# Performance work log

Hardware: AMD Instinct MI355X
Metric: run time of the kernel (lower is better)

The kernel has to match this reference:

```python
import jax, jax.numpy as jnp
import numpy as np
import math

# ---- static configuration (mirrors Renderer defaults) ----
S = 129                                 # density cube side
L = math.ceil(S * math.sqrt(3))         # padded/rotation cube side = 224
C_ABS = 0.2                             # absorption coefficient c
LIGHTS = [
    {'dir': (2, 1, 1),    'rgb': (1.0, 69.0 / 255.0, 25.0 / 255.0)},
    {'dir': (-1, 0.5, 0), 'rgb': (227.0 / 255.0, 1.0, 66.0 / 255.0)},
]


def yp_from_light(l):
    ld = np.asarray(l, dtype=np.float64)
    ld = ld / np.sqrt(np.sum(ld ** 2))
    y = -math.asin(ld[0])
    if ld[2] < 0:
        y = -math.pi - y
    y = y * 180.0 / math.pi
    p = math.asin(ld[1]) * 180.0 / math.pi
    return y, p


def rot_matrix(yaw_deg, pitch_deg, order):
    # yaw about the y (height) axis, pitch about the x axis, roll = 0
    y = math.radians(yaw_deg)
    p = math.radians(pitch_deg)
    Ry = np.array([[math.cos(y), 0.0, math.sin(y)],
                   [0.0, 1.0, 0.0],
                   [-math.sin(y), 0.0, math.cos(y)]], dtype=np.float32)
    Rp = np.array([[1.0, 0.0, 0.0],
                   [0.0, math.cos(p), -math.sin(p)],
                   [0.0, math.sin(p), math.cos(p)]], dtype=np.float32)
    return Ry @ Rp if order == 'ypr' else Rp @ Ry

# base normalized sampling grid (align_corners=True convention), (x,y,z) order
_lin = np.linspace(-1.0, 1.0, L, dtype=np.float32)
_zz, _yy, _xx = np.meshgrid(_lin, _lin, _lin, indexing='ij')
BASE_XYZ = np.stack([_xx, _yy, _zz], axis=-1)   # [L,L,L,3]


def rotate_volume(vol, R):
    """Trilinear resampling of vol [B,C,D,H,W] under rotation R (zero padding)."""
    B, Ch, D, H, W = vol.shape
    src = jnp.einsum('dhwc,kc->dhwk', jnp.asarray(BASE_XYZ), jnp.asarray(R))
    xs = (src[..., 0] + 1.0) * 0.5 * (W - 1)
    ys = (src[..., 1] + 1.0) * 0.5 * (H - 1)
    zs = (src[..., 2] + 1.0) * 0.5 * (D - 1)
    x0 = jnp.floor(xs).astype(jnp.int32)
    y0 = jnp.floor(ys).astype(jnp.int32)
    z0 = jnp.floor(zs).astype(jnp.int32)
    wx = (xs - x0).astype(vol.dtype)
    wy = (ys - y0).astype(vol.dtype)
    wz = (zs - z0).astype(vol.dtype)
    flat = vol.reshape(B, Ch, D * H * W)

    def gather(zi, yi, xi):
        inb = ((zi >= 0) & (zi < D) & (yi >= 0) & (yi < H) & (xi >= 0) & (xi < W)).astype(vol.dtype)
        idx = ((jnp.clip(zi, 0, D - 1) * H + jnp.clip(yi, 0, H - 1)) * W
               + jnp.clip(xi, 0, W - 1)).reshape(-1)
        return jnp.take(flat, idx, axis=2).reshape(B, Ch, D, H, W) * inb

    out = (gather(z0,     y0,     x0)     * ((1 - wz) * (1 - wy) * (1 - wx))
         + gather(z0,     y0,     x0 + 1) * ((1 - wz) * (1 - wy) * wx)
         + gather(z0,     y0 + 1, x0)     * ((1 - wz) * wy * (1 - wx))
         + gather(z0,     y0 + 1, x0 + 1) * ((1 - wz) * wy * wx)
         + gather(z0 + 1, y0,     x0)     * (wz * (1 - wy) * (1 - wx))
         + gather(z0 + 1, y0,     x0 + 1) * (wz * (1 - wy) * wx)
         + gather(z0 + 1, y0 + 1, x0)     * (wz * wy * (1 - wx))
         + gather(z0 + 1, y0 + 1, x0 + 1) * (wz * wy * wx))
    return out


def _revcumsum(a):
    # torch.flip(cumsum(flip(a,[2]),2),[2]) : reverse cumulative sum along depth
    return jnp.flip(jnp.cumsum(jnp.flip(a, 2), axis=2), 2)


def setup_inputs() -> dict:
    key = jax.random.key(0)
    d = jax.random.uniform(key, (1, 1, S, S, S), dtype=jnp.float32)
    return {'d': d}


def reference(d):
    bs, _, Sd, _, _ = d.shape
    i = L // 2 - Sd // 2
    j = i + Sd
    light_array = jnp.zeros((bs, 3, Sd, Sd, Sd), dtype=d.dtype)
    for l in LIGHTS:
        y, p = yp_from_light(l['dir'])
        up = jnp.zeros((bs, 1, L, L, L), dtype=d.dtype).at[:, :, i:j, i:j, i:j].set(d)
        up = rotate_volume(up, rot_matrix(y, p, 'ypr'))
        up = jnp.exp(-C_ABS * _revcumsum(up))           # transmittance toward light
        up = rotate_volume(up, rot_matrix(-y, -p, 'rpy'))
        color = jnp.asarray(l['rgb'], dtype=d.dtype).reshape(1, 3, 1, 1, 1)
        light_array = light_array + up[:, :, i:j, i:j, i:j] * color
    t = jnp.exp(-C_ABS * _revcumsum(d))                  # view-ray transmittance
    out = C_ABS * jnp.sum(d * light_array * t, axis=2)   # background = 0
    return jnp.clip(out, 0.0, 1.0)
```

## Files before the change

### kernel.cpp

```cpp
#include <hip/hip_runtime.h>
#include <hip/hip_fp16.h>
#include <math.h>

#ifndef M_PI
#define M_PI 3.14159265358979323846
#endif

#define SS   129
#define LL   224
#define LL2  (LL*LL)
#define LL3  (LL*LL*LL)
#define SS2  (SS*SS)
#define SS3  (SS*SS*SS)
#define CABS 0.2f
#define PAD  48

#define BLO 45.5f
#define BHI 178.5f

#define NT1  28
#define NTZ16 14
#define ROTG  (2 * NTZ16 * 784)
#define NT3  17
#define TPL3 4913
#define NTZ  28
#define NSEG 4
#define SEGZ 33

#define RBX 21
#define RBY 16
#define RBZ 18
#define RBN (RBX*RBY*RBZ)
#define RSXZ (RBX*RBZ)

#define GLN  3584

struct Mat3 { float m[9]; };
struct F3   { float x, y, z; };

__device__ __forceinline__ F3 tile_center(const Mat3& M, int ox, int oy, int oz) {
    float cbx = fmaf((float)ox + 3.5f, 2.0f / 223.0f, -1.0f);
    float cby = fmaf((float)oy + 3.5f, 2.0f / 223.0f, -1.0f);
    float cbz = fmaf((float)oz + 3.5f, 2.0f / 223.0f, -1.0f);
    F3 qc;
    qc.x = fmaf(fmaf(M.m[0], cbx, fmaf(M.m[1], cby, M.m[2] * cbz)), 111.5f, 111.5f);
    qc.y = fmaf(fmaf(M.m[3], cbx, fmaf(M.m[4], cby, M.m[5] * cbz)), 111.5f, 111.5f);
    qc.z = fmaf(fmaf(M.m[6], cbx, fmaf(M.m[7], cby, M.m[8] * cbz)), 111.5f, 111.5f);
    return qc;
}

__device__ __forceinline__ F3 tile_center16(const Mat3& M, int ox, int oy, int oz) {
    float cbx = fmaf((float)ox + 3.5f, 2.0f / 223.0f, -1.0f);
    float cby = fmaf((float)oy + 3.5f, 2.0f / 223.0f, -1.0f);
    float cbz = fmaf((float)oz + 7.5f, 2.0f / 223.0f, -1.0f);
    F3 qc;
    qc.x = fmaf(fmaf(M.m[0], cbx, fmaf(M.m[1], cby, M.m[2] * cbz)), 111.5f, 111.5f);
    qc.y = fmaf(fmaf(M.m[3], cbx, fmaf(M.m[4], cby, M.m[5] * cbz)), 111.5f, 111.5f);
    qc.z = fmaf(fmaf(M.m[6], cbx, fmaf(M.m[7], cby, M.m[8] * cbz)), 111.5f, 111.5f);
    return qc;
}

__device__ __forceinline__ bool tile_accept(F3 qc, F3 H) {
    return !(qc.x + H.x < BLO || qc.x - H.x > BHI ||
             qc.y + H.y < BLO || qc.y - H.y > BHI ||
             qc.z + H.z < BLO || qc.z - H.z > BHI);
}

__device__ __forceinline__ void qmap(const Mat3& M, int x, int y, int z,
                                     float& qx, float& qy, float& qz) {
    float bx = fmaf((float)x, 2.0f / 223.0f, -1.0f);
    float by = fmaf((float)y, 2.0f / 223.0f, -1.0f);
    float bz = fmaf((float)z, 2.0f / 223.0f, -1.0f);
    qx = fmaf(fmaf(M.m[0], bx, fmaf(M.m[1], by, M.m[2] * bz)), 111.5f, 111.5f);
    qy = fmaf(fmaf(M.m[3], bx, fmaf(M.m[4], by, M.m[5] * bz)), 111.5f, 111.5f);
    qz = fmaf(fmaf(M.m[6], bx, fmaf(M.m[7], by, M.m[8] * bz)), 111.5f, 111.5f);
}

__device__ __forceinline__ float fetch_d(const float* __restrict__ d, int z, int y, int x) {
    unsigned zz = (unsigned)(z - PAD), yy = (unsigned)(y - PAD), xx = (unsigned)(x - PAD);
    return (zz < (unsigned)SS && yy < (unsigned)SS && xx < (unsigned)SS)
        ? d[((int)zz * SS + (int)yy) * SS + (int)xx] : 0.0f;
}

__device__ __forceinline__ float fetch_T(const float* __restrict__ T, int z, int y, int x) {
    unsigned zz = (unsigned)z, yy = (unsigned)y, xx = (unsigned)x;
    return (zz < (unsigned)LL && yy < (unsigned)LL && xx < (unsigned)LL)
        ? T[((int)zz * LL + (int)yy) * LL + (int)xx] : 0.0f;
}

__device__ __forceinline__ float tri_T(const float* __restrict__ T, float qz, float qy, float qx) {
    int x0 = (int)floorf(qx), y0 = (int)floorf(qy), z0 = (int)floorf(qz);
    float wx = qx - (float)x0, wy = qy - (float)y0, wz = qz - (float)z0;
    float c000 = fetch_T(T, z0, y0, x0),     c001 = fetch_T(T, z0, y0, x0 + 1);
    float c010 = fetch_T(T, z0, y0 + 1, x0), c011 = fetch_T(T, z0, y0 + 1, x0 + 1);
    float c100 = fetch_T(T, z0 + 1, y0, x0),     c101 = fetch_T(T, z0 + 1, y0, x0 + 1);
    float c110 = fetch_T(T, z0 + 1, y0 + 1, x0), c111 = fetch_T(T, z0 + 1, y0 + 1, x0 + 1);
    float a00 = c000 + wx * (c001 - c000), a01 = c010 + wx * (c011 - c010);
    float a10 = c100 + wx * (c101 - c100), a11 = c110 + wx * (c111 - c110);
    float b0 = a00 + wy * (a01 - a00), b1 = a10 + wy * (a11 - a10);
    return b0 + wz * (b1 - b0);
}

__device__ __forceinline__ float tri_d_g(const float* __restrict__ d, float qz, float qy, float qx) {
    int x0 = (int)floorf(qx), y0 = (int)floorf(qy), z0 = (int)floorf(qz);
    float wx = qx - (float)x0, wy = qy - (float)y0, wz = qz - (float)z0;
    float c000 = fetch_d(d, z0, y0, x0),     c001 = fetch_d(d, z0, y0, x0 + 1);
    float c010 = fetch_d(d, z0, y0 + 1, x0), c011 = fetch_d(d, z0, y0 + 1, x0 + 1);
    float c100 = fetch_d(d, z0 + 1, y0, x0),     c101 = fetch_d(d, z0 + 1, y0, x0 + 1);
    float c110 = fetch_d(d, z0 + 1, y0 + 1, x0), c111 = fetch_d(d, z0 + 1, y0 + 1, x0 + 1);
    float a00 = c000 + wx * (c001 - c000), a01 = c010 + wx * (c011 - c010);
    float a10 = c100 + wx * (c101 - c100), a11 = c110 + wx * (c111 - c110);
    float b0 = a00 + wy * (a01 - a00), b1 = a10 + wy * (a11 - a10);
    return b0 + wz * (b1 - b0);
}

__device__ __forceinline__ float tri_rot(const float* __restrict__ S,
                                         float qx, float qy, float qz,
                                         int lox, int loy, int loz) {
    int x0 = (int)floorf(qx), y0 = (int)floorf(qy), z0 = (int)floorf(qz);
    float wx = qx - (float)x0, wy = qy - (float)y0, wz = qz - (float)z0;
    int i = (y0 - loy) * 378 + (z0 - loz) * 21 + (x0 - lox);
    float c000 = S[i],        c001 = S[i + 1];
    float cz0  = S[i + 21],   cz1  = S[i + 22];
    float cy0  = S[i + 378],  cy1  = S[i + 379];
    float cw0  = S[i + 399],  cw1  = S[i + 400];
    float a00 = c000 + wx * (c001 - c000);
    float a01 = cy0  + wx * (cy1  - cy0);
    float a10 = cz0  + wx * (cz1  - cz0);
    float a11 = cw0  + wx * (cw1  - cw0);
    float b0  = a00 + wy * (a01 - a00);
    float b1  = a10 + wy * (a11 - a10);
    return b0 + wz * (b1 - b0);
}

__device__ __forceinline__ float tri_back(const float* __restrict__ S,
                                          float qx, float qy, float qz,
                                          int lox, int loy, int loz) {
    int x0 = (int)floorf(qx), y0 = (int)floorf(qy), z0 = (int)floorf(qz);
    float wx = qx - (float)x0, wy = qy - (float)y0, wz = qz - (float)z0;
    int i = ((y0 - loy) * 16 + (z0 - loz)) * 16 + (x0 - lox);
    float c000 = S[i],       c001 = S[i + 1];
    float cz0  = S[i + 16],  cz1  = S[i + 17];
    float cy0  = S[i + 256], cy1  = S[i + 257];
    float cw0  = S[i + 272], cw1  = S[i + 273];
    float a00 = c000 + wx * (c001 - c000);
    float a01 = cy0  + wx * (cy1  - cy0);
    float a10 = cz0  + wx * (cz1  - cz0);
    float a11 = cw0  + wx * (cw1  - cw0);
    float b0  = a00 + wy * (a01 - a00);
    float b1  = a10 + wy * (a11 - a10);
    return b0 + wz * (b1 - b0);
}

__global__ __launch_bounds__(256) void k_pre(const float* __restrict__ d,
        float* __restrict__ Dseg, float* __restrict__ A,
        unsigned short* __restrict__ Run, Mat3 M0, Mat3 M1, F3 H0, F3 H1) {
    int b = blockIdx.x;
    if (b < 261) {
        int t = b * 256 + threadIdx.x;
        if (t < 2 * SS2) A[t] = 0.0f;
        if (t >= NSEG * SS2) return;
        int seg = t / SS2, col = t - seg * SS2;
        int zs = seg * SEGZ, ze = min(SS, zs + SEGZ);
        float run = 0.0f;
        for (int z = zs; z < ze; ++z) run += d[z * SS2 + col];
        Dseg[t] = run;
    } else {
        int id = (b - 261) * 256 + threadIdx.x;
        if (id >= 2 * 784) return;
        int l = id / 784, r = id - l * 784;
        int ty = r / 28, tx = r - ty * 28;
        const Mat3 M = l ? M1 : M0;
        const F3  H  = l ? H1 : H0;
        int t0 = -1, t1 = -1;
        for (int tz = 0; tz < NT1; ++tz) {
            F3 qc = tile_center(M, tx * 8, ty * 8, tz * 8);
            if (tile_accept(qc, H)) { if (t0 < 0) t0 = tz; t1 = tz; }
        }
        Run[id] = (t0 < 0) ? 0xFFFFu : (unsigned short)(t0 | (t1 << 8));
    }
}

__global__ __launch_bounds__(512) void k_rot(const float* __restrict__ d,
        __half* __restrict__ T0, __half* __restrict__ T1,
        float* __restrict__ S0, float* __restrict__ S1,
        Mat3 M0, Mat3 M1, F3 H0, F3 H1) {
    int b = blockIdx.x;
    int light = b / (NTZ16 * 784);
    int r = b - light * (NTZ16 * 784);
    int tz16 = r / 784;
    int r2 = r - tz16 * 784;
    int tty = r2 / 28, ttx = r2 - tty * 28;

    const Mat3 M = light ? M1 : M0;
    const F3  H  = light ? H1 : H0;
    __half* __restrict__ T   = light ? T1 : T0;
    float* __restrict__ Ssum = light ? S1 : S0;

    int ox = ttx * 8, oy = tty * 8, oz = tz16 * 16;
    F3 qc = tile_center16(M, ox, oy, oz);
    if (!tile_accept(qc, H)) return;

    int lox = (int)floorf(qc.x - H.x);
    int loy = (int)floorf(qc.y - H.y);
    int loz = (int)floorf(qc.z - H.z);

    __shared__ float S[RBN];
    __shared__ float Sc[1024];
    int tid = threadIdx.x;

    if (tid < RSXZ) {
        int ix = tid % RBX, iz = tid / RBX;
        int lb = iz * RBX + ix;
        bool interior = (lox >= PAD) & (lox <= PAD + SS - RBX) &
                        (loy >= PAD) & (loy <= PAD + SS - RBY) &
                        (loz >= PAD) & (loz <= PAD + SS - RBZ);
        if (interior) {
            const float* g = d + ((size_t)(loz + iz - PAD) * SS + (loy - PAD)) * SS
                               + (lox + ix - PAD);
            #pragma unroll
            for (int j = 0; j < RBY; ++j)
                S[lb + j * RSXZ] = g[j * SS];
        } else {
            #pragma unroll
            for (int j = 0; j < RBY; ++j)
                S[lb + j * RSXZ] = fetch_d(d, loz + iz, loy + j, lox + ix);
        }
    }
    __syncthreads();

    int lx = tid & 7, ly = (tid >> 3) & 7, lz = tid >> 6;
    int col = tid & 63;
    float fx = (float)lx - 3.5f, fy = (float)ly - 3.5f, fz = (float)lz - 7.5f;
    float qx = qc.x + fmaf(M.m[0], fx, fmaf(M.m[1], fy, M.m[2] * fz));
    float qy = qc.y + fmaf(M.m[3], fx, fmaf(M.m[4], fy, M.m[5] * fz));
    float qz = qc.z + fmaf(M.m[6], fx, fmaf(M.m[7], fy, M.m[8] * fz));
    float v0 = tri_rot(S, qx, qy, qz, lox, loy, loz);
    float qx2 = qx + 8.0f * M.m[2];
    float qy2 = qy + 8.0f * M.m[5];
    float qz2 = qz + 8.0f * M.m[8];
    float v1 = tri_rot(S, qx2, qy2, qz2, lox, loy, loz);

    Sc[lz * 64 + col] = v0;
    Sc[(lz + 8) * 64 + col] = v1;
    __syncthreads();
    if (tid < 64) {
        int so = (oy + (tid >> 3)) * LL + (ox + (tid & 7));
        float s = 0.0f;
        #pragma unroll
        for (int k = 15; k >= 8; --k) { s += Sc[k * 64 + tid]; Sc[k * 64 + tid] = s; }
        Ssum[(2 * tz16 + 1) * LL2 + so] = s;
        float s2 = 0.0f;
        #pragma unroll
        for (int k = 7; k >= 0; --k) { s2 += Sc[k * 64 + tid]; Sc[k * 64 + tid] = s2; }
        Ssum[(2 * tz16) * LL2 + so] = s2;
    }
    __syncthreads();
    int to = (oy + ly) * LL + (ox + lx);
    T[(size_t)(oz + lz) * LL2 + to]     = __float2half(Sc[lz * 64 + col]);
    T[(size_t)(oz + 8 + lz) * LL2 + to] = __float2half(Sc[(lz + 8) * 64 + col]);
}

__global__ __launch_bounds__(256) void k_sufw(float* __restrict__ S0,
        float* __restrict__ S1, const unsigned short* __restrict__ Run,
        const float* __restrict__ d, const float* __restrict__ Dseg,
        float* __restrict__ W) {
    int b = blockIdx.x;
    if (b < 392) {
        int l = b / 196;
        int col = (b - l * 196) * 256 + threadIdx.x;
        float* __restrict__ Ssum = l ? S1 : S0;
        int x = col % LL, y = col / LL;
        unsigned short r = Run[l * 784 + (y >> 3) * 28 + (x >> 3)];
        if (r == 0xFFFFu) return;
        int t0 = r & 0xFF, t1 = r >> 8;
        float vbuf[NTZ];
        #pragma unroll
        for (int t = 0; t < NTZ; ++t)
            vbuf[t] = (t >= t0 && t <= t1) ? Ssum[t * LL2 + col] : 0.0f;
        float run = 0.0f;
        #pragma unroll
        for (int t = NTZ - 1; t >= 0; --t) {
            if (t >= t0 && t <= t1) Ssum[t * LL2 + col] = run;
            run += vbuf[t];
        }
    } else {
        int t = (b - 392) * 256 + threadIdx.x;
        if (t >= NSEG * SS2) return;
        int seg = t / SS2, col = t - seg * SS2;
        int zs = seg * SEGZ, ze = min(SS, zs + SEGZ);
        float run = 0.0f;
        for (int s2 = seg + 1; s2 < NSEG; ++s2) run += Dseg[s2 * SS2 + col];
        for (int z = ze - 1; z >= zs; --z) {
            float dv = d[z * SS2 + col];
            run += dv;
            W[z * SS2 + col] = dv * __expf(-CABS * run);
        }
    }
}

template<bool BINT>
__global__ __launch_bounds__(512) void k_back(const __half* __restrict__ T0,
        const __half* __restrict__ T1, const float* __restrict__ S0,
        const float* __restrict__ S1, const float* __restrict__ W,
        float* __restrict__ A0, float* __restrict__ A1,
        Mat3 M0, Mat3 M1, F3 H0, F3 H1) {
    int b = blockIdx.x;
    int light = b / TPL3; b -= light * TPL3;
    const Mat3 M = light ? M1 : M0;
    const F3  H  = light ? H1 : H0;
    const __half* __restrict__ T   = light ? T1 : T0;
    const float* __restrict__ Ssum = light ? S1 : S0;
    float* __restrict__ A = light ? A1 : A0;

    int ttx = b % NT3; int rr = b / NT3; int tty = rr % NT3; int ttz = rr / NT3;
    int ox = ttx * 8, oy = tty * 8, oz = ttz * 8;
    F3 qc = tile_center(M, ox + PAD, oy + PAD, oz + PAD);
    int lox = (int)floorf(qc.x - H.x);
    int loy = (int)floorf(qc.y - H.y);
    int loz = (int)floorf(qc.z - H.z);

    __shared__ float S[GLN];
    __shared__ float Sc[512];
    int tid = threadIdx.x;
    int ix = tid & 15, iz = (tid >> 4) & 15, iy0 = tid >> 8;

    if (BINT) {
        int off = ((loz + iz) * LL + (loy + iy0)) * LL + (lox + ix);
        int sof = ((loz + iz) >> 3) * LL2 + (loy + iy0) * LL + (lox + ix);
        #pragma unroll
        for (int k = 0; k < 7; ++k)
            S[tid + k * 512] = __expf(-CABS * (__half2float(T[off + k * 2 * LL])
                                             + Ssum[sof + k * 2 * LL]));
    } else {
        #pragma unroll
        for (int k = 0; k < 7; ++k) {
            int gz = loz + iz, gy = loy + iy0 + 2 * k, gx = lox + ix;
            bool inb = ((unsigned)gz < (unsigned)LL) & ((unsigned)gy < (unsigned)LL)
                     & ((unsigned)gx < (unsigned)LL);
            float e = 0.0f;
            if (inb)
                e = __expf(-CABS * (__half2float(T[(gz * LL + gy) * LL + gx])
                                  + Ssum[(gz >> 3) * LL2 + gy * LL + gx]));
            S[tid + k * 512] = e;
        }
    }
    __syncthreads();

    int lx = tid & 7, ly = (tid >> 3) & 7, lz = tid >> 6;
    int x = ox + lx, y = oy + ly, z = oz + lz;
    float v = 0.0f;
    if (x < SS && y < SS && z < SS) {
        float fx = (float)lx - 3.5f, fy = (float)ly - 3.5f, fz = (float)lz - 3.5f;
        float qx = qc.x + fmaf(M.m[0], fx, fmaf(M.m[1], fy, M.m[2] * fz));
        float qy = qc.y + fmaf(M.m[3], fx, fmaf(M.m[4], fy, M.m[5] * fz));
        float qz = qc.z + fmaf(M.m[6], fx, fmaf(M.m[7], fy, M.m[8] * fz));
        float u = tri_back(S, qx, qy, qz, lox, loy, loz);
        v = u * W[(z * SS + y) * SS + x];
    }
    Sc[tid] = v;
    __syncthreads();
    if (tid < 64) {
        float s = 0.0f;
        #pragma unroll
        for (int k = 0; k < 8; ++k) s += Sc[tid + 64 * k];
        int xx = ox + (tid & 7), yy = oy + (tid >> 3);
        if (xx < SS && yy < SS) atomicAdd(&A[yy * SS + xx], s);
    }
}

__global__ __launch_bounds__(256) void k_combine(const float* __restrict__ A0,
        const float* __restrict__ A1, float* __restrict__ out, F3 c0, F3 c1) {
    int i = blockIdx.x * 256 + threadIdx.x;
    if (i >= 3 * SS2) return;
    int ch = i / SS2, col = i - ch * SS2;
    float r0 = (ch == 0) ? c0.x : ((ch == 1) ? c0.y : c0.z);
    float r1 = (ch == 0) ? c1.x : ((ch == 1) ? c1.y : c1.z);
    float o = CABS * (A0[col] * r0 + A1[col] * r1);
    out[i] = fminf(fmaxf(o, 0.0f), 1.0f);
}

__global__ __launch_bounds__(256) void k_rot_full(const float* __restrict__ d,
                                                  float* __restrict__ T, Mat3 R) {
    int i = blockIdx.x * 256 + threadIdx.x;
    if (i >= LL3) return;
    int x = i % LL; int r = i / LL; int y = r % LL; int z = r / LL;
    float qx, qy, qz; qmap(R, x, y, z, qx, qy, qz);
    T[i] = tri_d_g(d, qz, qy, qx);
}

__global__ __launch_bounds__(256) void k_scan_full(float* __restrict__ T) {
    int col = blockIdx.x * 256 + threadIdx.x;
    if (col >= LL2) return;
    float run = 0.0f;
    for (int z = LL - 1; z >= 0; --z) {
        int idx = z * LL2 + col;
        run += T[idx];
        T[idx] = __expf(-CABS * run);
    }
}

__global__ __launch_bounds__(64) void k_fused_back(const float* __restrict__ T,
        const float* __restrict__ d, float* __restrict__ LA, Mat3 RT,
        float cr, float cg, float cb, int first) {
    int col = blockIdx.x * 64 + threadIdx.x;
    if (col >= SS2) return;
    int y = col / SS, x = col % SS;
    float run = 0.0f, acc = 0.0f;
    for (int z = SS - 1; z >= 0; --z) {
        float qx, qy, qz; qmap(RT, x + PAD, y + PAD, z + PAD, qx, qy, qz);
        float u = tri_T(T, qz, qy, qx);
        float dv = d[z * SS2 + col];
        run += dv;
        acc = fmaf(dv * __expf(-CABS * run), u, acc);
    }
    if (first) {
        LA[0 * SS2 + col] = acc * cr;
        LA[1 * SS2 + col] = acc * cg;
        LA[2 * SS2 + col] = acc * cb;
    } else {
        LA[0 * SS2 + col] += acc * cr;
        LA[1 * SS2 + col] += acc * cg;
        LA[2 * SS2 + col] += acc * cb;
    }
}

__global__ __launch_bounds__(256) void k_clip(const float* __restrict__ LA,
                                              float* __restrict__ out) {
    int i = blockIdx.x * 256 + threadIdx.x;
    if (i < 3 * SS2) out[i] = fminf(fmaxf(CABS * LA[i], 0.0f), 1.0f);
}

static void light_mats(const double ld_in[3], Mat3& R, Mat3& RT) {
    double n = sqrt(ld_in[0]*ld_in[0] + ld_in[1]*ld_in[1] + ld_in[2]*ld_in[2]);
    double l0 = ld_in[0]/n, l1 = ld_in[1]/n, l2 = ld_in[2]/n;
    double yv = -asin(l0);
    if (l2 < 0) yv = -M_PI - yv;
    double yd = yv * 180.0 / M_PI, pd = asin(l1) * 180.0 / M_PI;
    double yr = yd * M_PI / 180.0, pr = pd * M_PI / 180.0;
    float cy = (float)cos(yr), sy = (float)sin(yr), cp = (float)cos(pr), sp = (float)sin(pr);
    float m[9] = { cy,  sy*sp,  sy*cp,
                   0.f, cp,    -sp,
                  -sy,  cy*sp,  cy*cp };
    for (int i = 0; i < 9; ++i) R.m[i] = m[i];
    RT.m[0] = m[0]; RT.m[1] = m[3]; RT.m[2] = m[6];
    RT.m[3] = m[1]; RT.m[4] = m[4]; RT.m[5] = m[7];
    RT.m[6] = m[2]; RT.m[7] = m[5]; RT.m[8] = m[8];
}

static F3 half_span8(const Mat3& M) {
    F3 h;
    h.x = 3.5f * (fabsf(M.m[0]) + fabsf(M.m[1]) + fabsf(M.m[2])) + 0.05f;
    h.y = 3.5f * (fabsf(M.m[3]) + fabsf(M.m[4]) + fabsf(M.m[5])) + 0.05f;
    h.z = 3.5f * (fabsf(M.m[6]) + fabsf(M.m[7]) + fabsf(M.m[8])) + 0.05f;
    return h;
}

static F3 half_span16(const Mat3& M) {
    F3 h;
    h.x = 3.5f * (fabsf(M.m[0]) + fabsf(M.m[1])) + 7.5f * fabsf(M.m[2]) + 0.1f;
    h.y = 3.5f * (fabsf(M.m[3]) + fabsf(M.m[4])) + 7.5f * fabsf(M.m[5]) + 0.1f;
    h.z = 3.5f * (fabsf(M.m[6]) + fabsf(M.m[7])) + 7.5f * fabsf(M.m[8]) + 0.1f;
    return h;
}

static void h_qc(const Mat3& M, double ox, double oy, double oz, double q[3]) {
    double cb[3] = { (ox + 3.5) * 2.0 / 223.0 - 1.0,
                     (oy + 3.5) * 2.0 / 223.0 - 1.0,
                     (oz + 3.5) * 2.0 / 223.0 - 1.0 };
    for (int k = 0; k < 3; ++k)
        q[k] = ((double)M.m[3*k] * cb[0] + (double)M.m[3*k+1] * cb[1]
              + (double)M.m[3*k+2] * cb[2]) * 111.5 + 111.5;
}

extern "C" void kernel_launch(void* const* d_in, const int* in_sizes, int n_in,
                              void* d_out, int out_size, void* d_ws, size_t ws_size,
                              hipStream_t stream) {
    const float* d = (const float*)d_in[0];
    float* out = (float*)d_out;

    const double dirs[2][3] = { {2.0, 1.0, 1.0}, {-1.0, 0.5, 0.0} };
    F3 c0 = { 1.0f, 69.0f / 255.0f, 25.0f / 255.0f };
    F3 c1 = { 227.0f / 255.0f, 1.0f, 66.0f / 255.0f };
    Mat3 R[2], RT[2];
    light_mats(dirs[0], R[0], RT[0]);
    light_mats(dirs[1], R[1], RT[1]);
    F3 H8[2]  = { half_span8(R[0]),  half_span8(R[1])  };
    F3 H16[2] = { half_span16(R[0]), half_span16(R[1]) };
    F3 HB[2]  = { half_span8(RT[0]), half_span8(RT[1]) };

    bool bint = true;
    for (int l = 0; l < 2 && bint; ++l) {
        double H[3] = { HB[l].x, HB[l].y, HB[l].z };
        int dim[3] = { 16, 14, 16 };
        for (int tz = 0; tz < NT3 && bint; ++tz)
            for (int ty = 0; ty < NT3 && bint; ++ty)
                for (int tx = 0; tx < NT3; ++tx) {
                    double q[3]; h_qc(RT[l], tx * 8 + PAD, ty * 8 + PAD, tz * 8 + PAD, q);
                    for (int k = 0; k < 3; ++k) {
                        int lo = (int)floor(q[k] - H[k]);
                        if (lo < 1 || lo + dim[k] > LL - 1) { bint = false; break; }
                    }
                    if (!bint) break;
                }
    }

    const size_t f32n = (size_t)(2 * NTZ * LL2 + SS3 + NSEG * SS2 + 2 * SS2);
    const size_t need_A = f32n * 4 + (size_t)2 * LL3 * 2 + 2 * 784 * 2;
    const size_t need_C = (size_t)(LL3 + 3 * SS2) * 4;

    if (ws_size >= need_A) {
        float* S0   = (float*)d_ws;
        float* S1   = S0 + NTZ * LL2;
        float* W    = S1 + NTZ * LL2;
        float* Dseg = W + SS3;
        float* A0   = Dseg + NSEG * SS2;
        float* A1   = A0 + SS2;
        __half* T0  = (__half*)(A1 + SS2);
        __half* T1  = T0 + LL3;
        unsigned short* Run = (unsigned short*)(T1 + LL3);

        k_pre  <<<268, 256, 0, stream>>>(d, Dseg, A0, Run, R[0], R[1], H8[0], H8[1]);
        k_rot  <<<ROTG, 512, 0, stream>>>(d, T0, T1, S0, S1, R[0], R[1], H16[0], H16[1]);
        k_sufw <<<653, 256, 0, stream>>>(S0, S1, Run, d, Dseg, W);
        if (bint)
            k_back<true><<<2 * TPL3, 512, 0, stream>>>(T0, T1, S0, S1, W, A0, A1,
                                                       RT[0], RT[1], HB[0], HB[1]);
        else
            k_back<false><<<2 * TPL3, 512, 0, stream>>>(T0, T1, S0, S1, W, A0, A1,
                                                        RT[0], RT[1], HB[0], HB[1]);
        k_combine<<<(3 * SS2 + 255) / 256, 256, 0, stream>>>(A0, A1, out, c0, c1);
    } else if (ws_size >= need_C) {
        float* T  = (float*)d_ws;
        float* LA = T + LL3;
        for (int l = 0; l < 2; ++l) {
            k_rot_full <<<(LL3 + 255) / 256, 256, 0, stream>>>(d, T, R[l]);
            k_scan_full<<<(LL2 + 255) / 256, 256, 0, stream>>>(T);
            k_fused_back<<<(SS2 + 63) / 64, 64, 0, stream>>>(T, d, LA, RT[l],
                l ? c1.x : c0.x, l ? c1.y : c0.y, l ? c1.z : c0.z, l == 0);
        }
        k_clip<<<(3 * SS2 + 255) / 256, 256, 0, stream>>>(LA, out);
    }
}
```

Measured before the change: 178.7 us.

## Use 8x8x16 tiles in back-projection and skip rot tiles via precomputed runs

The back-projection kernel now processes 8x8x16 output tiles with 512 threads, two samples per thread, instead of 8x8x8 tiles. Each block loads one larger 21x16x19 shared-memory neighbourhood of exponentiated transmittance, which halves the block count and the number of atomicAdd reductions into the accumulator. The rotation kernel now culls empty tiles with the per-column run table already computed in k_pre, replacing its own per-block tile_accept test. The cost is fewer blocks per launch and more shared memory per block, which may reduce occupancy. It also relies on the coarser 8-deep run bounds being a conservative stand-in for the 16-deep tile acceptance.

Measured after the change: 180.7 us. About the same (+1.1%).

```diff
diff --git a/kernel.cpp b/kernel.cpp
--- a/kernel.cpp
+++ b/kernel.cpp
@@ -22,7 +22,8 @@
 #define NTZ16 14
 #define ROTG  (2 * NTZ16 * 784)
 #define NT3  17
-#define TPL3 4913
+#define NBZ16 9
+#define BACKG (2 * NBZ16 * 289)
 #define NTZ  28
 #define NSEG 4
 #define SEGZ 33
@@ -33,7 +34,11 @@
 #define RBN (RBX*RBY*RBZ)
 #define RSXZ (RBX*RBZ)
 
-#define GLN  3584
+#define BBX 21
+#define BBY 16
+#define BBZ 19
+#define BBN (BBX*BBY*BBZ)
+#define BSXZ (BBX*BBZ)
 
 struct Mat3 { float m[9]; };
 struct F3   { float x, y, z; };
@@ -138,11 +143,11 @@
                                           int lox, int loy, int loz) {
     int x0 = (int)floorf(qx), y0 = (int)floorf(qy), z0 = (int)floorf(qz);
     float wx = qx - (float)x0, wy = qy - (float)y0, wz = qz - (float)z0;
-    int i = ((y0 - loy) * 16 + (z0 - loz)) * 16 + (x0 - lox);
-    float c000 = S[i],       c001 = S[i + 1];
-    float cz0  = S[i + 16],  cz1  = S[i + 17];
-    float cy0  = S[i + 256], cy1  = S[i + 257];
-    float cw0  = S[i + 272], cw1  = S[i + 273];
+    int i = (y0 - loy) * 399 + (z0 - loz) * 21 + (x0 - lox);
+    float c000 = S[i],        c001 = S[i + 1];
+    float cz0  = S[i + 21],   cz1  = S[i + 22];
+    float cy0  = S[i + 399],  cy1  = S[i + 400];
+    float cw0  = S[i + 420],  cw1  = S[i + 421];
     float a00 = c000 + wx * (c001 - c000);
     float a01 = cy0  + wx * (cy1  - cy0);
     float a10 = cz0  + wx * (cz1  - cz0);
@@ -184,6 +189,7 @@
 __global__ __launch_bounds__(512) void k_rot(const float* __restrict__ d,
         __half* __restrict__ T0, __half* __restrict__ T1,
         float* __restrict__ S0, float* __restrict__ S1,
+        const unsigned short* __restrict__ Run,
         Mat3 M0, Mat3 M1, F3 H0, F3 H1) {
     int b = blockIdx.x;
     int light = b / (NTZ16 * 784);
@@ -192,6 +198,11 @@
     int r2 = r - tz16 * 784;
     int tty = r2 / 28, ttx = r2 - tty * 28;
 
+    unsigned short rt = Run[light * 784 + tty * 28 + ttx];
+    if (rt == 0xFFFFu) return;
+    int t0 = rt & 0xFF, t1 = rt >> 8;
+    if (2 * tz16 + 1 < t0 || 2 * tz16 > t1) return;
+
     const Mat3 M = light ? M1 : M0;
     const F3  H  = light ? H1 : H0;
     __half* __restrict__ T   = light ? T1 : T0;
@@ -199,7 +210,6 @@
 
     int ox = ttx * 8, oy = tty * 8, oz = tz16 * 16;
     F3 qc = tile_center16(M, ox, oy, oz);
-    if (!tile_accept(qc, H)) return;
 
     int lox = (int)floorf(qc.x - H.x);
     int loy = (int)floorf(qc.y - H.y);
@@ -211,7 +221,6 @@
 
     if (tid < RSXZ) {
         int ix = tid % RBX, iz = tid / RBX;
-        int lb = iz * RBX + ix;
         bool interior = (lox >= PAD) & (lox <= PAD + SS - RBX) &
                         (loy >= PAD) & (loy <= PAD + SS - RBY) &
                         (loz >= PAD) & (loz <= PAD + SS - RBZ);
@@ -220,11 +229,11 @@
                                + (lox + ix - PAD);
             #pragma unroll
             for (int j = 0; j < RBY; ++j)
-                S[lb + j * RSXZ] = g[j * SS];
+                S[tid + j * RSXZ] = g[j * SS];
         } else {
             #pragma unroll
             for (int j = 0; j < RBY; ++j)
-                S[lb + j * RSXZ] = fetch_d(d, loz + iz, loy + j, lox + ix);
+                S[tid + j * RSXZ] = fetch_d(d, loz + iz, loy + j, lox + ix);
         }
     }
     __syncthreads();
@@ -306,64 +315,77 @@
         float* __restrict__ A0, float* __restrict__ A1,
         Mat3 M0, Mat3 M1, F3 H0, F3 H1) {
     int b = blockIdx.x;
-    int light = b / TPL3; b -= light * TPL3;
+    int light = b / (NBZ16 * 289); b -= light * (NBZ16 * 289);
+    int tz16 = b / 289;
+    int r2 = b - tz16 * 289;
+    int tty = r2 / 17, ttx = r2 - tty * 17;
+
     const Mat3 M = light ? M1 : M0;
     const F3  H  = light ? H1 : H0;
     const __half* __restrict__ T   = light ? T1 : T0;
     const float* __restrict__ Ssum = light ? S1 : S0;
     float* __restrict__ A = light ? A1 : A0;
 
-    int ttx = b % NT3; int rr = b / NT3; int tty = rr % NT3; int ttz = rr / NT3;
-    int ox = ttx * 8, oy = tty * 8, oz = ttz * 8;
-    F3 qc = tile_center(M, ox + PAD, oy + PAD, oz + PAD);
+    int ox = ttx * 8, oy = tty * 8, oz = tz16 * 16;
+    F3 qc = tile_center16(M, ox + PAD, oy + PAD, oz + PAD);
     int lox = (int)floorf(qc.x - H.x);
     int loy = (int)floorf(qc.y - H.y);
     int loz = (int)floorf(qc.z - H.z);
 
-    __shared__ float S[GLN];
-    __shared__ float Sc[512];
+    __shared__ float S[BBN];
+    __shared__ float Sc[1024];
     int tid = threadIdx.x;
-    int ix = tid & 15, iz = (tid >> 4) & 15, iy0 = tid >> 8;
-
-    if (BINT) {
-        int off = ((loz + iz) * LL + (loy + iy0)) * LL + (lox + ix);
-        int sof = ((loz + iz) >> 3) * LL2 + (loy + iy0) * LL + (lox + ix);
-        #pragma unroll
-        for (int k = 0; k < 7; ++k)
-            S[tid + k * 512] = __expf(-CABS * (__half2float(T[off + k * 2 * LL])
-                                             + Ssum[sof + k * 2 * LL]));
-    } else {
-        #pragma unroll
-        for (int k = 0; k < 7; ++k) {
-            int gz = loz + iz, gy = loy + iy0 + 2 * k, gx = lox + ix;
-            bool inb = ((unsigned)gz < (unsigned)LL) & ((unsigned)gy < (unsigned)LL)
-                     & ((unsigned)gx < (unsigned)LL);
-            float e = 0.0f;
-            if (inb)
-                e = __expf(-CABS * (__half2float(T[(gz * LL + gy) * LL + gx])
-                                  + Ssum[(gz >> 3) * LL2 + gy * LL + gx]));
-            S[tid + k * 512] = e;
+
+    if (tid < BSXZ) {
+        int ix = tid % BBX, iz = tid / BBX;
+        if (BINT) {
+            const __half* tb = T + ((size_t)(loz + iz) * LL + loy) * LL + (lox + ix);
+            const float* sb = Ssum + (size_t)((loz + iz) >> 3) * LL2 + loy * LL + (lox + ix);
+            #pragma unroll
+            for (int j = 0; j < BBY; ++j)
+                S[tid + j * BSXZ] = __expf(-CABS * (__half2float(tb[j * LL]) + sb[j * LL]));
+        } else {
+            #pragma unroll
+            for (int j = 0; j < BBY; ++j) {
+                int gz = loz + iz, gy = loy + j, gx = lox + ix;
+                bool inb = ((unsigned)gz < (unsigned)LL) & ((unsigned)gy < (unsigned)LL)
+                         & ((unsigned)gx < (unsigned)LL);
+                float e = 0.0f;
+                if (inb)
+                    e = __expf(-CABS * (__half2float(T[((size_t)gz * LL + gy) * LL + gx])
+                                      + Ssum[(size_t)(gz >> 3) * LL2 + gy * LL + gx]));
+                S[tid + j * BSXZ] = e;
+            }
         }
     }
     __syncthreads();
 
     int lx = tid & 7, ly = (tid >> 3) & 7, lz = tid >> 6;
-    int x = ox + lx, y = oy + ly, z = oz + lz;
-    float v = 0.0f;
-    if (x < SS && y < SS && z < SS) {
-        float fx = (float)lx - 3.5f, fy = (float)ly - 3.5f, fz = (float)lz - 3.5f;
+    int col = tid & 63;
+    int x = ox + lx, y = oy + ly;
+    float v0 = 0.0f, v1 = 0.0f;
+    if (x < SS && y < SS) {
+        float fx = (float)lx - 3.5f, fy = (float)ly - 3.5f, fz = (float)lz - 7.5f;
         float qx = qc.x + fmaf(M.m[0], fx, fmaf(M.m[1], fy, M.m[2] * fz));
         float qy = qc.y + fmaf(M.m[3], fx, fmaf(M.m[4], fy, M.m[5] * fz));
         float qz = qc.z + fmaf(M.m[6], fx, fmaf(M.m[7], fy, M.m[8] * fz));
-        float u = tri_back(S, qx, qy, qz, lox, loy, loz);
-        v = u * W[(z * SS + y) * SS + x];
-    }
-    Sc[tid] = v;
+        int z0 = oz + lz, z1 = oz + 8 + lz;
+        if (z0 < SS)
+            v0 = tri_back(S, qx, qy, qz, lox, loy, loz) * W[(z0 * SS + y) * SS + x];
+        if (z1 < SS) {
+            float qx2 = qx + 8.0f * M.m[2];
+            float qy2 = qy + 8.0f * M.m[5];
+            float qz2 = qz + 8.0f * M.m[8];
+            v1 = tri_back(S, qx2, qy2, qz2, lox, loy, loz) * W[(z1 * SS + y) * SS + x];
+        }
+    }
+    Sc[lz * 64 + col] = v0;
+    Sc[(lz + 8) * 64 + col] = v1;
     __syncthreads();
     if (tid < 64) {
         float s = 0.0f;
         #pragma unroll
-        for (int k = 0; k < 8; ++k) s += Sc[tid + 64 * k];
+        for (int k = 0; k < 16; ++k) s += Sc[k * 64 + tid];
         int xx = ox + (tid & 7), yy = oy + (tid >> 3);
         if (xx < SS && yy < SS) atomicAdd(&A[yy * SS + xx], s);
     }
@@ -464,10 +486,10 @@
     return h;
 }
 
-static void h_qc(const Mat3& M, double ox, double oy, double oz, double q[3]) {
+static void h_qc16(const Mat3& M, double ox, double oy, double oz, double q[3]) {
     double cb[3] = { (ox + 3.5) * 2.0 / 223.0 - 1.0,
                      (oy + 3.5) * 2.0 / 223.0 - 1.0,
-                     (oz + 3.5) * 2.0 / 223.0 - 1.0 };
+                     (oz + 7.5) * 2.0 / 223.0 - 1.0 };
     for (int k = 0; k < 3; ++k)
         q[k] = ((double)M.m[3*k] * cb[0] + (double)M.m[3*k+1] * cb[1]
               + (double)M.m[3*k+2] * cb[2]) * 111.5 + 111.5;
@@ -487,16 +509,16 @@
     light_mats(dirs[1], R[1], RT[1]);
     F3 H8[2]  = { half_span8(R[0]),  half_span8(R[1])  };
     F3 H16[2] = { half_span16(R[0]), half_span16(R[1]) };
-    F3 HB[2]  = { half_span8(RT[0]), half_span8(RT[1]) };
+    F3 HB[2]  = { half_span16(RT[0]), half_span16(RT[1]) };
 
     bool bint = true;
     for (int l = 0; l < 2 && bint; ++l) {
         double H[3] = { HB[l].x, HB[l].y, HB[l].z };
-        int dim[3] = { 16, 14, 16 };
-        for (int tz = 0; tz < NT3 && bint; ++tz)
+        int dim[3] = { BBX, BBY, BBZ };
+        for (int tz = 0; tz < NBZ16 && bint; ++tz)
             for (int ty = 0; ty < NT3 && bint; ++ty)
                 for (int tx = 0; tx < NT3; ++tx) {
-                    double q[3]; h_qc(RT[l], tx * 8 + PAD, ty * 8 + PAD, tz * 8 + PAD, q);
+                    double q[3]; h_qc16(RT[l], tx * 8 + PAD, ty * 8 + PAD, tz * 16 + PAD, q);
                     for (int k = 0; k < 3; ++k) {
                         int lo = (int)floor(q[k] - H[k]);
                         if (lo < 1 || lo + dim[k] > LL - 1) { bint = false; break; }
@@ -521,14 +543,15 @@
         unsigned short* Run = (unsigned short*)(T1 + LL3);
 
         k_pre  <<<268, 256, 0, stream>>>(d, Dseg, A0, Run, R[0], R[1], H8[0], H8[1]);
-        k_rot  <<<ROTG, 512, 0, stream>>>(d, T0, T1, S0, S1, R[0], R[1], H16[0], H16[1]);
+        k_rot  <<<ROTG, 512, 0, stream>>>(d, T0, T1, S0, S1, Run,
+                                          R[0], R[1], H16[0], H16[1]);
         k_sufw <<<653, 256, 0, stream>>>(S0, S1, Run, d, Dseg, W);
         if (bint)
-            k_back<true><<<2 * TPL3, 512, 0, stream>>>(T0, T1, S0, S1, W, A0, A1,
-                                                       RT[0], RT[1], HB[0], HB[1]);
+            k_back<true><<<BACKG, 512, 0, stream>>>(T0, T1, S0, S1, W, A0, A1,
+                                                    RT[0], RT[1], HB[0], HB[1]);
         else
-            k_back<false><<<2 * TPL3, 512, 0, stream>>>(T0, T1, S0, S1, W, A0, A1,
-                                                        RT[0], RT[1], HB[0], HB[1]);
+            k_back<false><<<BACKG, 512, 0, stream>>>(T0, T1, S0, S1, W, A0, A1,
+                                                     RT[0], RT[1], HB[0], HB[1]);
         k_combine<<<(3 * SS2 + 255) / 256, 256, 0, stream>>>(A0, A1, out, c0, c1);
     } else if (ws_size >= need_C) {
         float* T  = (float*)d_ws;
```
